# Optimization experiments

Hardware: AMD Instinct MI355X
Metric: run time of the kernel (lower is better)

The kernel has to match this reference:

```python
import jax, jax.numpy as jnp
import numpy as np

QK_NOPE = 128
QK_ROPE = 64
V_DIM = 128
N_HEADS = 16
ROPE_BASE = 10000.0
RMS_EPS = 1e-6


def _rms_norm(x, w, eps=RMS_EPS):
    x = x.astype(jnp.float32)
    var = jnp.mean(x * x, axis=-1, keepdims=True)
    return w * x * jax.lax.rsqrt(var + eps)


def _rotate_half(x):
    x1, x2 = jnp.split(x, 2, axis=-1)
    return jnp.concatenate([-x2, x1], axis=-1)


def _rope_cos_sin(position_ids, dim=QK_ROPE, base=ROPE_BASE):
    # factor=1.0 YaRN collapses to plain RoPE with mscale=1
    inv_freq = 1.0 / (base ** (jnp.arange(0, dim, 2, dtype=jnp.float32) / dim))
    freqs = position_ids.astype(jnp.float32)[..., None] * inv_freq  # [B,S,dim/2]
    emb = jnp.concatenate([freqs, freqs], axis=-1)                  # [B,S,dim]
    return jnp.cos(emb), jnp.sin(emb)


def setup_inputs() -> dict:
    key = jax.random.key(0)
    ks = jax.random.split(key, 8)
    B, S, H = 1, 2048, 4096
    q_lora, kv_lora = 1536, 512
    q_head = QK_NOPE + QK_ROPE
    s = lambda k, shp, fan: jax.random.normal(k, shp, jnp.float32) * (fan ** -0.5)
    return {
        "hidden_states": jax.random.normal(ks[0], (B, S, H), jnp.float32),
        "position_ids": jnp.broadcast_to(jnp.arange(S, dtype=jnp.int64), (B, S)),
        "wq_a": s(ks[1], (q_lora, H), H),
        "q_a_norm_w": jnp.ones((q_lora,), jnp.float32),
        "wq_b": s(ks[2], (N_HEADS * q_head, q_lora), q_lora),
        "wkv_a": s(ks[3], (kv_lora + QK_ROPE, H), H),
        "kv_a_norm_w": jnp.ones((kv_lora,), jnp.float32),
        "wkv_b": s(ks[4], (N_HEADS * (QK_NOPE + V_DIM), kv_lora), kv_lora),
        "wo": s(ks[5], (H, N_HEADS * V_DIM), N_HEADS * V_DIM),
    }


def reference(hidden_states, position_ids, wq_a, q_a_norm_w, wq_b, wkv_a,
              kv_a_norm_w, wkv_b, wo):
    B, S, _ = hidden_states.shape
    kv_lora = kv_a_norm_w.shape[0]
    q_head = QK_NOPE + QK_ROPE
    softmax_scale = q_head ** -0.5  # mscale_all_dim=0 -> no yarn correction

    # Q low-rank path
    q_lat = _rms_norm(hidden_states @ wq_a.T, q_a_norm_w).astype(hidden_states.dtype)
    q = (q_lat @ wq_b.T).reshape(B, S, N_HEADS, q_head)
    q_nope, q_pe = q[..., :QK_NOPE], q[..., QK_NOPE:]

    # KV low-rank path
    kv = hidden_states @ wkv_a.T
    compressed_kv = _rms_norm(kv[..., :kv_lora], kv_a_norm_w).astype(hidden_states.dtype)
    k_pe = kv[..., kv_lora:].reshape(B, S, 1, QK_ROPE)

    cos, sin = _rope_cos_sin(position_ids)
    cos_h, sin_h = cos[:, :, None, :], sin[:, :, None, :]
    q_pe = q_pe * cos_h + _rotate_half(q_pe) * sin_h
    k_pe = k_pe * cos_h + _rotate_half(k_pe) * sin_h

    kv_exp = (compressed_kv @ wkv_b.T).reshape(B, S, N_HEADS, QK_NOPE + V_DIM)
    k_nope, v = kv_exp[..., :QK_NOPE], kv_exp[..., QK_NOPE:]

    qf = jnp.concatenate([q_nope, q_pe], axis=-1).astype(jnp.float32)   # [B,S,H,Dq]
    kf = jnp.concatenate([k_nope, jnp.broadcast_to(k_pe, (B, S, N_HEADS, QK_ROPE))],
                         axis=-1).astype(jnp.float32)
    vf = v.astype(jnp.float32)

    scores = jnp.einsum('bqhd,bkhd->bhqk', qf, kf) * softmax_scale
    causal = jnp.tril(jnp.ones((S, S), dtype=bool))
    scores = jnp.where(causal, scores, -jnp.inf)
    probs = jax.nn.softmax(scores, axis=-1)
    out = jnp.einsum('bhqk,bkhd->bqhd', probs, vf).astype(hidden_states.dtype)
    out = out.reshape(B, S, N_HEADS * V_DIM)
    return out @ wo.T
```

## Files before the change

### kernel.cpp

```cpp
#include <hip/hip_runtime.h>
#include <hip/hip_bf16.h>


typedef short bf16x8 __attribute__((ext_vector_type(8)));
typedef float f32x4  __attribute__((ext_vector_type(4)));

#if __has_builtin(__builtin_amdgcn_global_load_lds)
#define USE_GLL 1
#else
#define USE_GLL 0
#endif

__device__ __forceinline__ void stage16(const void* g, void* l) {
#if USE_GLL
    __builtin_amdgcn_global_load_lds(
        (__attribute__((address_space(1))) void*)(g),
        (__attribute__((address_space(3))) void*)(l), 16, 0, 0);
#else
    *(uint4*)l = *(const uint4*)g;
#endif
}

#define LOG2E 1.4426950408889634f

__device__ __forceinline__ short bf16_bits(float v) {
    union { __hip_bfloat16 h; short s; } u;
    u.h = __float2bfloat16(v);
    return u.s;
}

__global__ __launch_bounds__(256)
void cvt_bf16(const float* __restrict__ s, __hip_bfloat16* __restrict__ d, int nq) {
    int i = blockIdx.x * 256 + threadIdx.x;
    if (i >= nq) return;
    float4 v = ((const float4*)s)[i];
    union { uint2 u; __hip_bfloat16 h[4]; } r;
    r.h[0] = __float2bfloat16(v.x); r.h[1] = __float2bfloat16(v.y);
    r.h[2] = __float2bfloat16(v.z); r.h[3] = __float2bfloat16(v.w);
    ((uint2*)d)[i] = r.u;
}

__global__ __launch_bounds__(256)
void zero_f32(float* __restrict__ p, int n4) {
    int i = blockIdx.x * 256 + threadIdx.x;
    if (i < n4) ((float4*)p)[i] = float4{0.f, 0.f, 0.f, 0.f};
}

__global__ __launch_bounds__(256)
void zero_u4(uint4* __restrict__ p, int n) {
    int i = blockIdx.x * 256 + threadIdx.x;
    if (i < n) p[i] = make_uint4(0u, 0u, 0u, 0u);
}

__global__ __launch_bounds__(256)
void kpe_copy(const float* __restrict__ fused, float* __restrict__ kpe) {
    int i = blockIdx.x * 256 + threadIdx.x;
    int r = i >> 6, c = i & 63;
    kpe[i] = fused[(size_t)r * 2112 + 2048 + c];
}

template<int OUTMODE>
__global__ __launch_bounds__(256)
void gemm_lds(const __hip_bfloat16* __restrict__ A,
              const __hip_bfloat16* __restrict__ B,
              void* __restrict__ C,
              int K, int Cld, int Nlim, int ksteps) {
    __shared__ __align__(16) short As[128 * 64];
    __shared__ __align__(16) short Bs[128 * 64];

    const int tid  = threadIdx.x;
    const int lane = tid & 63;
    const int wave = tid >> 6;
    const int quad = lane >> 4;
    const int l16  = lane & 15;
    const int m0 = blockIdx.y * 128;
    const int n0 = blockIdx.x * 128;
    const int wm = (wave >> 1) * 64;
    const int wn = (wave & 1) * 64;
    const int kbeg = blockIdx.z * ksteps * 64;

    const int lrow = lane >> 3;
    const int lchk = lane & 7;
    const int sb   = (lchk ^ lrow) * 16;

    f32x4 acc[4][4];
    #pragma unroll
    for (int i = 0; i < 4; i++)
        #pragma unroll
        for (int j = 0; j < 4; j++)
            acc[i][j] = f32x4{0.f, 0.f, 0.f, 0.f};

    const size_t str = (size_t)K * 2;
    const char* Ab = (const char*)A;
    const char* Bb = (const char*)B;

    for (int kk = 0; kk < ksteps; kk++) {
        if (kk) __syncthreads();
        const size_t koff = (size_t)(kbeg + kk * 64) * 2;
        #pragma unroll
        for (int t = 0; t < 4; t++) {
            const int row = wave * 32 + t * 8 + lrow;
            stage16(Ab + (size_t)(m0 + row) * str + koff + sb,
                    (char*)As + row * 128 + lchk * 16);
            stage16(Bb + (size_t)(n0 + row) * str + koff + sb,
                    (char*)Bs + row * 128 + lchk * 16);
        }
        __syncthreads();

        #pragma unroll
        for (int ks = 0; ks < 2; ks++) {
            const int ca = ((ks * 4 + quad) ^ (l16 & 7)) * 8;
            bf16x8 af[4], bfr[4];
            #pragma unroll
            for (int mi = 0; mi < 4; mi++)
                af[mi] = *(const bf16x8*)(&As[(wm + mi * 16 + l16) * 64 + ca]);
            #pragma unroll
            for (int ni = 0; ni < 4; ni++)
                bfr[ni] = *(const bf16x8*)(&Bs[(wn + ni * 16 + l16) * 64 + ca]);
            #pragma unroll
            for (int mi = 0; mi < 4; mi++)
                #pragma unroll
                for (int ni = 0; ni < 4; ni++)
                    acc[mi][ni] = __builtin_amdgcn_mfma_f32_16x16x32_bf16(
                        af[mi], bfr[ni], acc[mi][ni], 0, 0, 0);
        }
    }

    #pragma unroll
    for (int mi = 0; mi < 4; mi++)
        #pragma unroll
        for (int ni = 0; ni < 4; ni++) {
            const int col = n0 + wn + ni * 16 + l16;
            if (col >= Nlim) continue;
            #pragma unroll
            for (int r = 0; r < 4; r++) {
                const int row = m0 + wm + mi * 16 + quad * 4 + r;
                const float v = acc[mi][ni][r];
                if (OUTMODE == 0)
                    ((__hip_bfloat16*)C)[(size_t)row * Cld + col] = __float2bfloat16(v);
                else if (OUTMODE == 1)
                    ((float*)C)[(size_t)row * Cld + col] = v;
                else
                    atomicAdd(&((float*)C)[(size_t)row * Cld + col], v);
            }
        }
}

__global__ __launch_bounds__(256)
void rmsnorm_k(const float* __restrict__ X, const float* __restrict__ w,
               __hip_bfloat16* __restrict__ Y, int W, int sx, int sy) {
    int row = blockIdx.x;
    const float* x = X + (size_t)row * sx;
    float ss = 0.f;
    for (int i = threadIdx.x; i < W; i += 256) { float v = x[i]; ss += v * v; }
    for (int off = 32; off; off >>= 1) ss += __shfl_down(ss, off);
    __shared__ float red[4];
    int lane = threadIdx.x & 63, wv = threadIdx.x >> 6;
    if (lane == 0) red[wv] = ss;
    __syncthreads();
    float tot = red[0] + red[1] + red[2] + red[3];
    float inv = rsqrtf(tot / (float)W + 1e-6f);
    for (int i = threadIdx.x; i < W; i += 256) {
        float v = x[i] * inv * w[i];
        Y[(size_t)row * sy + i] = __float2bfloat16(v);
    }
}

__global__ __launch_bounds__(256)
void rope_assemble(__hip_bfloat16* __restrict__ q,
                   const __hip_bfloat16* __restrict__ kvexp,
                   const float* __restrict__ kpe_in,
                   __hip_bfloat16* __restrict__ kfT) {
    int s = blockIdx.x;
    int tid = threadIdx.x;
    __shared__ float cs[32], sn[32];
    __shared__ __hip_bfloat16 kpe[64];
    if (tid < 32) {
        float inv = expf(-(float)tid * (logf(10000.0f) / 32.0f));
        float ang = (float)s * inv;
        cs[tid] = cosf(ang);
        sn[tid] = sinf(ang);
    }
    __syncthreads();
    if (tid < 32) {
        float x1 = kpe_in[(size_t)s * 64 + tid];
        float x2 = kpe_in[(size_t)s * 64 + 32 + tid];
        kpe[tid]      = __float2bfloat16(x1 * cs[tid] - x2 * sn[tid]);
        kpe[tid + 32] = __float2bfloat16(x2 * cs[tid] + x1 * sn[tid]);
    }
    for (int p = tid; p < 512; p += 256) {
        int h = p >> 5, j = p & 31;
        size_t base = (size_t)s * 3072 + h * 192 + 128;
        float x1 = __bfloat162float(q[base + j]);
        float x2 = __bfloat162float(q[base + j + 32]);
        q[base + j]      = __float2bfloat16(x1 * cs[j] - x2 * sn[j]);
        q[base + j + 32] = __float2bfloat16(x2 * cs[j] + x1 * sn[j]);
    }
    __syncthreads();
    for (int i = tid; i < 16 * 192; i += 256) {
        int h = i / 192, d = i % 192;
        __hip_bfloat16 v = (d < 128) ? kvexp[(size_t)s * 4096 + h * 256 + d]
                                     : kpe[d - 128];
        kfT[((size_t)(h * 24 + (d >> 3)) * 2048 + s) * 8 + (d & 7)] = v;
    }
}

__global__ __launch_bounds__(256)
void transpose_v(const __hip_bfloat16* __restrict__ kvexp,
                 __hip_bfloat16* __restrict__ vT2) {
    __shared__ short t[64 * 72];
    int s0 = blockIdx.x * 64, d0 = blockIdx.y * 64, h = blockIdx.z;
    int c = threadIdx.x & 63;
    int r4 = threadIdx.x >> 6;
    for (int i = 0; i < 16; i++) {
        int r = r4 * 16 + i;
        t[r * 72 + c] = *(const short*)&kvexp[(size_t)(s0 + r) * 4096 + h * 256 + 128 + d0 + c];
    }
    __syncthreads();
    for (int it = 0; it < 2; it++) {
        int scl = it * 4 + (threadIdx.x >> 6);
        int d   = threadIdx.x & 63;
        union { uint4 u; short sh[8]; } pk;
        #pragma unroll
        for (int e = 0; e < 8; e++) pk.sh[e] = t[(scl * 8 + e) * 72 + d];
        size_t cell = ((size_t)h * 256 + blockIdx.x * 8 + scl) * 128 + d0 + d;
        ((uint4*)vT2)[cell] = pk.u;
    }
}

__global__ __launch_bounds__(256, 3)
void attn_kernel(const __hip_bfloat16* __restrict__ qb,
                 const __hip_bfloat16* __restrict__ kfT,
                 const __hip_bfloat16* __restrict__ vT2,
                 __hip_bfloat16* __restrict__ out) {
    const int h  = blockIdx.y;
    const int qt = 31 - blockIdx.x;
    const int q0 = qt * 64;
    const int tid  = threadIdx.x;
    const int wave = tid >> 6;
    const int lane = tid & 63;
    const int quad = lane >> 4;
    const int l16  = lane & 15;

    __shared__ __align__(16) short Ks2[24 * 64 * 8];
    __shared__ __align__(16) short Vs2[ 8 * 128 * 8];
    __shared__ __align__(16) short Ps2[ 8 * 64 * 8];

    const float scale = 0.07216878364870322f;

    bf16x8 qfr[6];
    {
        int row = q0 + wave * 16 + l16;
        const __hip_bfloat16* qrow = qb + ((size_t)row * 16 + h) * 192;
        for (int ks = 0; ks < 6; ks++) {
            union { bf16x8 v; __hip_bfloat16 h8[8]; } u;
            u.v = *(const bf16x8*)(qrow + ks * 32 + quad * 8);
            #pragma unroll
            for (int e = 0; e < 8; e++)
                u.h8[e] = __float2bfloat16(__bfloat162float(u.h8[e]) * scale);
            qfr[ks] = u.v;
        }
    }

    f32x4 o_acc[8];
    #pragma unroll
    for (int i = 0; i < 8; i++) o_acc[i] = f32x4{0.f, 0.f, 0.f, 0.f};
    float m_i[4], l_i[4];
    #pragma unroll
    for (int r = 0; r < 4; r++) { m_i[r] = -__builtin_inff(); l_i[r] = 0.f; }

    const char* kfb = (const char*)kfT;
    const char* vtb = (const char*)vT2;

    for (int kt = 0; kt <= qt; kt++) {
        if (kt) __syncthreads();
        #pragma unroll
        for (int j = 0; j < 6; j++) {
            int c = wave * 6 + j;
            stage16(kfb + (((size_t)(h * 24 + c) * 2048) + kt * 64 + lane) * 16,
                    (char*)Ks2 + (c * 64 + lane) * 16);
        }
        #pragma unroll
        for (int j = 0; j < 4; j++) {
            int c  = wave * 2 + (j >> 1);
            int hd = j & 1;
            stage16(vtb + (((size_t)(h * 256 + kt * 8 + c) * 128) + hd * 64 + lane) * 16,
                    (char*)Vs2 + (c * 128 + hd * 64 + lane) * 16);
        }
        __syncthreads();

        f32x4 sc[4];
        #pragma unroll
        for (int n = 0; n < 4; n++) sc[n] = f32x4{0.f, 0.f, 0.f, 0.f};
        #pragma unroll
        for (int ks = 0; ks < 6; ks++)
            #pragma unroll
            for (int n = 0; n < 4; n++) {
                bf16x8 kb = *(const bf16x8*)(&Ks2[((ks * 4 + quad) * 64 + n * 16 + l16) * 8]);
                sc[n] = __builtin_amdgcn_mfma_f32_16x16x32_bf16(qfr[ks], kb, sc[n], 0, 0, 0);
            }

        const bool last = (kt == qt);
        float tmax[4], rsum[4], alpha[4];
        #pragma unroll
        for (int r = 0; r < 4; r++) tmax[r] = -__builtin_inff();
        #pragma unroll
        for (int n = 0; n < 4; n++)
            #pragma unroll
            for (int r = 0; r < 4; r++) {
                float v = sc[n][r];
                if (last && (kt * 64 + n * 16 + l16) > (q0 + wave * 16 + quad * 4 + r))
                    v = -__builtin_inff();
                sc[n][r] = v;
                tmax[r] = fmaxf(tmax[r], v);
            }
        #pragma unroll
        for (int r = 0; r < 4; r++)
            #pragma unroll
            for (int off = 1; off < 16; off <<= 1)
                tmax[r] = fmaxf(tmax[r], __shfl_xor(tmax[r], off));
        #pragma unroll
        for (int r = 0; r < 4; r++) {
            float mn = fmaxf(m_i[r], tmax[r]);
            alpha[r] = exp2f((m_i[r] - mn) * LOG2E);
            m_i[r] = mn;
            rsum[r] = 0.f;
        }
        #pragma unroll
        for (int n = 0; n < 4; n++)
            #pragma unroll
            for (int r = 0; r < 4; r++) {
                float p = exp2f((sc[n][r] - m_i[r]) * LOG2E);
                sc[n][r] = p;
                rsum[r] += p;
            }
        #pragma unroll
        for (int r = 0; r < 4; r++) {
            #pragma unroll
            for (int off = 1; off < 16; off <<= 1)
                rsum[r] += __shfl_xor(rsum[r], off);
            l_i[r] = l_i[r] * alpha[r] + rsum[r];
        }
        #pragma unroll
        for (int n = 0; n < 4; n++)
            #pragma unroll
            for (int r = 0; r < 4; r++)
                Ps2[((n * 2 + (l16 >> 3)) * 64 + wave * 16 + quad * 4 + r) * 8 + (l16 & 7)] =
                    bf16_bits(sc[n][r]);
        #pragma unroll
        for (int d = 0; d < 8; d++)
            #pragma unroll
            for (int r = 0; r < 4; r++)
                o_acc[d][r] *= alpha[r];
        #pragma unroll
        for (int ks2 = 0; ks2 < 2; ks2++) {
            bf16x8 pa = *(const bf16x8*)(&Ps2[((ks2 * 4 + quad) * 64 + wave * 16 + l16) * 8]);
            #pragma unroll
            for (int dg = 0; dg < 8; dg++) {
                bf16x8 vb = *(const bf16x8*)(&Vs2[((ks2 * 4 + quad) * 128 + dg * 16 + l16) * 8]);
                o_acc[dg] = __builtin_amdgcn_mfma_f32_16x16x32_bf16(pa, vb, o_acc[dg], 0, 0, 0);
            }
        }
    }

    #pragma unroll
    for (int dg = 0; dg < 8; dg++)
        #pragma unroll
        for (int r = 0; r < 4; r++) {
            int row = q0 + wave * 16 + quad * 4 + r;
            float v = o_acc[dg][r] / l_i[r];
            out[((size_t)row * 16 + h) * 128 + dg * 16 + l16] = __float2bfloat16(v);
        }
}

extern "C" void kernel_launch(void* const* d_in, const int* in_sizes, int n_in,
                              void* d_out, int out_size, void* d_ws, size_t ws_size,
                              hipStream_t stream) {
    const float* hidden = (const float*)d_in[0];
    const float* wq_a   = (const float*)d_in[2];
    const float* q_a_w  = (const float*)d_in[3];
    const float* wq_b   = (const float*)d_in[4];
    const float* wkv_a  = (const float*)d_in[5];
    const float* kv_a_w = (const float*)d_in[6];
    const float* wkv_b  = (const float*)d_in[7];
    const float* wo     = (const float*)d_in[8];
    float* out = (float*)d_out;

    char* ws = (char*)d_ws;
    __hip_bfloat16* hiddenB = (__hip_bfloat16*)(ws + 0);
    __hip_bfloat16* wq_bB   = (__hip_bfloat16*)(ws + 0);
    __hip_bfloat16* kfT     = (__hip_bfloat16*)(ws + 0);
    __hip_bfloat16* W0      = (__hip_bfloat16*)(ws + 16777216);
    __hip_bfloat16* kv_exp  = (__hip_bfloat16*)(ws + 16777216);
    __hip_bfloat16* attn_o  = (__hip_bfloat16*)(ws + 16777216);
    float*          fused   = (float*)(ws + 34603008);
    __hip_bfloat16* qb      = (__hip_bfloat16*)(ws + 34603008);
    __hip_bfloat16* woB     = (__hip_bfloat16*)(ws + 34603008);
    __hip_bfloat16* wkv_bB  = (__hip_bfloat16*)(ws + 47185920);
    float*          kpe     = (float*)(ws + 51904512);
    __hip_bfloat16* q_lat   = (__hip_bfloat16*)(ws + 52428800);
    __hip_bfloat16* vT2     = (__hip_bfloat16*)(ws + 52428800);
    __hip_bfloat16* ckv     = (__hip_bfloat16*)(ws + 58720256);

    dim3 blk(256);
    cvt_bf16<<<8192, blk, 0, stream>>>(hidden, hiddenB, 2097152);
    cvt_bf16<<<6144, blk, 0, stream>>>(wq_a,  W0,               1572864);
    cvt_bf16<<<2304, blk, 0, stream>>>(wkv_a, W0 + 1536 * 4096,  589824);
    zero_u4<<<128, blk, 0, stream>>>((uint4*)(W0 + 2112 * 4096), 32768);
    zero_f32<<<4224, blk, 0, stream>>>(fused, 1081344);
    gemm_lds<2><<<dim3(17, 16, 4), blk, 0, stream>>>(hiddenB, W0, fused, 4096, 2112, 2112, 16);
    kpe_copy<<<512, blk, 0, stream>>>(fused, kpe);
    rmsnorm_k<<<2048, blk, 0, stream>>>(fused,        q_a_w,  q_lat, 1536, 2112, 1536);
    rmsnorm_k<<<2048, blk, 0, stream>>>(fused + 1536, kv_a_w, ckv,    512, 2112,  512);
    cvt_bf16<<<4608, blk, 0, stream>>>(wq_b,  wq_bB,  1179648);
    cvt_bf16<<<2048, blk, 0, stream>>>(wkv_b, wkv_bB,  524288);
    gemm_lds<0><<<dim3(24, 16), blk, 0, stream>>>(q_lat, wq_bB,  qb,     1536, 3072, 3072, 24);
    gemm_lds<0><<<dim3(32, 16), blk, 0, stream>>>(ckv,   wkv_bB, kv_exp,  512, 4096, 4096,  8);
    rope_assemble<<<2048, blk, 0, stream>>>(qb, kv_exp, kpe, kfT);
    transpose_v<<<dim3(32, 2, 16), blk, 0, stream>>>(kv_exp, vT2);
    attn_kernel<<<dim3(32, 16), blk, 0, stream>>>(qb, kfT, vT2, attn_o);
    cvt_bf16<<<8192, blk, 0, stream>>>(wo, woB, 2097152);
    gemm_lds<1><<<dim3(32, 16), blk, 0, stream>>>(attn_o, woB, out, 2048, 4096, 4096, 32);
}
```

Before: 479.7 us.

## Prefetch next K/V tile into registers and remap attention grid ordering

Replaces the direct global-to-LDS staging of the K and V tiles with register prefetch. The next tile's global loads are issued right after the barrier, so their latency overlaps the current tile's MFMA and softmax work. The launch grid also becomes 1D: the first 256 blocks take short causal query tiles (0..15) for each head and the next 256 take long ones (31..16), which changes the scheduling order. This adds register pressure (10 uint4 per thread) that may reduce occupancy under launch_bounds(256,3). The ordering change may hurt load balance, since the long tiles now launch last.

```diff
diff --git a/kernel.cpp b/kernel.cpp
--- a/kernel.cpp
+++ b/kernel.cpp
@@ -233,9 +233,13 @@
                  const __hip_bfloat16* __restrict__ kfT,
                  const __hip_bfloat16* __restrict__ vT2,
                  __hip_bfloat16* __restrict__ out) {
-    const int h  = blockIdx.y;
-    const int qt = 31 - blockIdx.x;
-    const int q0 = qt * 64;
+    const int b   = blockIdx.x;
+    const int p   = b & 255;
+    const int hi  = b >> 8;
+    const int h   = p >> 4;
+    const int j4  = p & 15;
+    const int qt  = hi ? (31 - j4) : j4;
+    const int q0  = qt * 64;
     const int tid  = threadIdx.x;
     const int wave = tid >> 6;
     const int lane = tid & 63;
@@ -247,6 +251,25 @@
     __shared__ __align__(16) short Ps2[ 8 * 64 * 8];
 
     const float scale = 0.07216878364870322f;
+
+    const char* kfb = (const char*)kfT;
+    const char* vtb = (const char*)vT2;
+
+    const char* kp0[6];
+    #pragma unroll
+    for (int j = 0; j < 6; j++)
+        kp0[j] = kfb + (((size_t)(h * 24 + wave * 6 + j) * 2048) + lane) * 16;
+    const char* vp0[4];
+    #pragma unroll
+    for (int j = 0; j < 4; j++)
+        vp0[j] = vtb + (((size_t)(h * 256 + wave * 2 + (j >> 1)) * 128)
+                        + (j & 1) * 64 + lane) * 16;
+
+    uint4 kr[6], vr[4];
+    #pragma unroll
+    for (int j = 0; j < 6; j++) kr[j] = *(const uint4*)(kp0[j]);
+    #pragma unroll
+    for (int j = 0; j < 4; j++) vr[j] = *(const uint4*)(vp0[j]);
 
     bf16x8 qfr[6];
     {
@@ -269,25 +292,25 @@
     #pragma unroll
     for (int r = 0; r < 4; r++) { m_i[r] = -__builtin_inff(); l_i[r] = 0.f; }
 
-    const char* kfb = (const char*)kfT;
-    const char* vtb = (const char*)vT2;
-
     for (int kt = 0; kt <= qt; kt++) {
         if (kt) __syncthreads();
         #pragma unroll
-        for (int j = 0; j < 6; j++) {
-            int c = wave * 6 + j;
-            stage16(kfb + (((size_t)(h * 24 + c) * 2048) + kt * 64 + lane) * 16,
-                    (char*)Ks2 + (c * 64 + lane) * 16);
-        }
-        #pragma unroll
-        for (int j = 0; j < 4; j++) {
-            int c  = wave * 2 + (j >> 1);
-            int hd = j & 1;
-            stage16(vtb + (((size_t)(h * 256 + kt * 8 + c) * 128) + hd * 64 + lane) * 16,
-                    (char*)Vs2 + (c * 128 + hd * 64 + lane) * 16);
-        }
+        for (int j = 0; j < 6; j++)
+            *(uint4*)((char*)Ks2 + ((wave * 6 + j) * 64 + lane) * 16) = kr[j];
+        #pragma unroll
+        for (int j = 0; j < 4; j++)
+            *(uint4*)((char*)Vs2 + ((wave * 2 + (j >> 1)) * 128
+                                    + (j & 1) * 64 + lane) * 16) = vr[j];
         __syncthreads();
+
+        if (kt < qt) {
+            const int koff = (kt + 1) * 1024;
+            const int voff = (kt + 1) * 16384;
+            #pragma unroll
+            for (int j = 0; j < 6; j++) kr[j] = *(const uint4*)(kp0[j] + koff);
+            #pragma unroll
+            for (int j = 0; j < 4; j++) vr[j] = *(const uint4*)(vp0[j] + voff);
+        }
 
         f32x4 sc[4];
         #pragma unroll
@@ -330,9 +353,9 @@
         for (int n = 0; n < 4; n++)
             #pragma unroll
             for (int r = 0; r < 4; r++) {
-                float p = exp2f((sc[n][r] - m_i[r]) * LOG2E);
-                sc[n][r] = p;
-                rsum[r] += p;
+                float p2 = exp2f((sc[n][r] - m_i[r]) * LOG2E);
+                sc[n][r] = p2;
+                rsum[r] += p2;
             }
         #pragma unroll
         for (int r = 0; r < 4; r++) {
@@ -418,7 +441,7 @@
     gemm_lds<0><<<dim3(32, 16), blk, 0, stream>>>(ckv,   wkv_bB, kv_exp,  512, 4096, 4096,  8);
     rope_assemble<<<2048, blk, 0, stream>>>(qb, kv_exp, kpe, kfT);
     transpose_v<<<dim3(32, 2, 16), blk, 0, stream>>>(kv_exp, vT2);
-    attn_kernel<<<dim3(32, 16), blk, 0, stream>>>(qb, kfT, vT2, attn_o);
+    attn_kernel<<<dim3(512), blk, 0, stream>>>(qb, kfT, vT2, attn_o);
     cvt_bf16<<<8192, blk, 0, stream>>>(wo, woB, 2097152);
     gemm_lds<1><<<dim3(32, 16), blk, 0, stream>>>(attn_o, woB, out, 2048, 4096, 4096, 32);
 }
```

New measurement: 568.2 us. 1.18x slower.
